# Kernel tuning notes

Hardware: AMD Instinct MI355X
Metric: run time of the kernel (lower is better)

Reference implementation:

```python
import math
import jax, jax.numpy as jnp
import numpy as np

WINDOW = 2  # LocalAttention default window_size
EPS = 1e-6


def _linear(x, W, b):
    return x @ W + b


def local_attention(x, Wq, bq, Wk, bk, Wv, bv):
    # x: [B, S, D]
    B, S, D = x.shape
    q = _linear(x, Wq, bq)
    k = _linear(x, Wk, bk)
    v = _linear(x, Wv, bv)
    idx = jnp.arange(S)
    # 0/1 banded mask -> softmax gives a dense row-stochastic matrix (faithful to source)
    mask = (jnp.abs(idx[:, None] - idx[None, :]) <= WINDOW).astype(x.dtype)  # [S, S]
    A = jax.nn.softmax(mask, axis=-1)  # [S, S]
    kk = jnp.einsum('st,btd->bsd', A, k)  # bmm(A, k)
    scores = jnp.einsum('bsd,btd->bst', q, kk) / math.sqrt(D)
    return jnp.einsum('bst,btd->bsd', jax.nn.softmax(scores, axis=-1), v)


def whole_norm(x, w, b):
    # LayerNorm with normalized_shape == full [B, S, D]: normalize over ALL elements
    mu = jnp.mean(x)
    var = jnp.mean(jnp.square(x - mu))
    return (x - mu) * jax.lax.rsqrt(var + EPS) * w + b


def ffn(x, W1, b1, W2, b2):
    return _linear(jax.nn.relu(_linear(x, W1, b1)), W2, b2)


def branch(feat, Wq, bq, Wk, bk, Wv, bv, W1, b1, W2, b2, nw, nb):
    out = local_attention(feat, Wq, bq, Wk, bk, Wv, bv)
    out = whole_norm(out + feat, nw, nb)
    out = ffn(out, W1, b1, W2, b2)
    return whole_norm(out + feat, nw, nb)


def _make_params(key, B, S, D):
    ks = jax.random.split(key, 5)
    s = 1.0 / math.sqrt(D)
    Wq = jax.random.normal(ks[0], (D, D), jnp.float32) * s
    Wk = jax.random.normal(ks[1], (D, D), jnp.float32) * s
    Wv = jax.random.normal(ks[2], (D, D), jnp.float32) * s
    W1 = jax.random.normal(ks[3], (D, 4 * D), jnp.float32) * s
    W2 = jax.random.normal(ks[4], (4 * D, D), jnp.float32) * (1.0 / math.sqrt(4 * D))
    return dict(Wq=Wq, bq=jnp.zeros((D,)), Wk=Wk, bk=jnp.zeros((D,)),
                Wv=Wv, bv=jnp.zeros((D,)), W1=W1, b1=jnp.zeros((4 * D,)),
                W2=W2, b2=jnp.zeros((D,)), nw=jnp.ones((B, S, D)), nb=jnp.zeros((B, S, D)))


def setup_inputs() -> dict:
    key = jax.random.key(0)
    k0, k1, k2, k3 = jax.random.split(key, 4)
    B, St, Dt = 8, 512, 1024
    Si, Di = 196, 768
    inp = {
        'text_feature': jax.random.normal(k0, (B, St, Dt), jnp.float32),
        'image_feature': jax.random.normal(k1, (B, Si, Di), jnp.float32),
    }
    tp = _make_params(k2, B, St, Dt)
    ip = _make_params(k3, B, Si, Di)
    for k, v in tp.items():
        inp['t_' + k] = v
    for k, v in ip.items():
        inp['i_' + k] = v
    return inp


def reference(text_feature, image_feature,
              t_Wq, t_bq, t_Wk, t_bk, t_Wv, t_bv, t_W1, t_b1, t_W2, t_b2, t_nw, t_nb,
              i_Wq, i_bq, i_Wk, i_bk, i_Wv, i_bv, i_W1, i_b1, i_W2, i_b2, i_nw, i_nb):
    image_out = branch(image_feature, i_Wq, i_bq, i_Wk, i_bk, i_Wv, i_bv,
                       i_W1, i_b1, i_W2, i_b2, i_nw, i_nb)
    text_out = branch(text_feature, t_Wq, t_bq, t_Wk, t_bk, t_Wv, t_bv,
                      t_W1, t_b1, t_W2, t_b2, t_nw, t_nb)
    return (text_out, image_out)
```

## Files before the change

### kernel.cpp

```cpp
#include <hip/hip_runtime.h>
#include <math.h>

typedef float  f32x4  __attribute__((ext_vector_type(4)));
typedef short  bf16x8 __attribute__((ext_vector_type(8)));

__device__ __forceinline__ unsigned short f2bf(float f) {
    union { float f; unsigned u; } v; v.f = f;
    unsigned u = v.u;
    return (unsigned short)((u + 0x7FFFu + ((u >> 16) & 1u)) >> 16);
}
__device__ __forceinline__ float bf2f(unsigned short u) {
    union { unsigned u; float f; } v; v.u = (unsigned)u << 16; return v.f;
}

#define GLOAD_LDS16(g, l)                                                      \
    __builtin_amdgcn_global_load_lds(                                          \
        (const __attribute__((address_space(1))) void*)(g),                    \
        (__attribute__((address_space(3))) void*)(l), 16, 0, 0)

template<int MR, int NR, bool OUT_BF16, bool RELU>
__global__ __launch_bounds__(512, 4)
void gemm2_bf16(const unsigned short* __restrict__ A,
                const unsigned short* __restrict__ BT,
                const float* __restrict__ bias, void* __restrict__ Cv,
                int M, int N, int K, int lda, int ldb, int ldc,
                long long sA, long long sB, long long sC, float alpha,
                int gx, int gy)
{
    constexpr int BK = 32;
    constexpr int WM = MR * 16, WN = NR * 16;
    constexpr int BM = 2 * WM, BN = 4 * WN;
    __shared__ unsigned short Asm[2][BM * BK];
    __shared__ unsigned short Bsm[2][BN * BK];

    A  += (long long)blockIdx.z * sA;
    BT += (long long)blockIdx.z * sB;
    char* Cb = (char*)Cv + (long long)blockIdx.z * sC * (OUT_BF16 ? 2 : 4);

    const int nwg = gx * gy;
    int orig = blockIdx.x;
    int xcd = orig & 7, sidx = orig >> 3;
    int qq = nwg >> 3, rr = nwg & 7;
    int wg = (xcd < rr ? xcd * (qq + 1) : rr * (qq + 1) + (xcd - rr) * qq) + sidx;
    const int row0 = (wg / gx) * BM;
    const int col0 = (wg % gx) * BN;

    const int tid  = threadIdx.x;
    const int lane = tid & 63;
    const int wave = tid >> 6;
    const int wr   = wave >> 2;
    const int wc   = wave & 3;

    const int srow = tid >> 2;
    const int skel = (tid & 3) * 8;

    const int lrow = lane & 15;
    const int lk   = (lane >> 4) * 8;

    f32x4 acc[MR][NR] = {};

    auto stage = [&](int buf, int k0) {
        #pragma unroll
        for (int is = 0; is < BM / 128; ++is)
            GLOAD_LDS16(A + (long long)(row0 + is * 128 + srow) * lda + (k0 + skel),
                        &Asm[buf][(is * 128 + srow) * BK + skel]);
        #pragma unroll
        for (int is = 0; is < BN / 128; ++is)
            GLOAD_LDS16(BT + (long long)(col0 + is * 128 + srow) * ldb + (k0 + skel),
                        &Bsm[buf][(is * 128 + srow) * BK + skel]);
    };

    const int nt = K / BK;
    stage(0, 0);
    __syncthreads();
    int cur = 0;
    for (int t = 0; t < nt; ++t) {
        if (t + 1 < nt) stage(cur ^ 1, (t + 1) * BK);

        bf16x8 af[MR], bfr[NR];
        #pragma unroll
        for (int mf = 0; mf < MR; ++mf)
            af[mf] = *(const bf16x8*)&Asm[cur][(wr * WM + mf * 16 + lrow) * BK + lk];
        #pragma unroll
        for (int nf = 0; nf < NR; ++nf)
            bfr[nf] = *(const bf16x8*)&Bsm[cur][(wc * WN + nf * 16 + lrow) * BK + lk];
        #pragma unroll
        for (int mf = 0; mf < MR; ++mf)
            #pragma unroll
            for (int nf = 0; nf < NR; ++nf)
                acc[mf][nf] = __builtin_amdgcn_mfma_f32_16x16x32_bf16(
                    af[mf], bfr[nf], acc[mf][nf], 0, 0, 0);

        __syncthreads();
        cur ^= 1;
    }

    const int crow = (lane >> 4) * 4;
    const int ccol = lane & 15;
    #pragma unroll
    for (int mf = 0; mf < MR; ++mf) {
        int rbase = row0 + wr * WM + mf * 16 + crow;
        #pragma unroll
        for (int nf = 0; nf < NR; ++nf) {
            int c = col0 + wc * WN + nf * 16 + ccol;
            if (c >= N) continue;
            float bv = bias ? bias[c] : 0.f;
            #pragma unroll
            for (int j = 0; j < 4; ++j) {
                int r = rbase + j;
                if (r >= M) continue;
                float v = acc[mf][nf][j] * alpha + bv;
                if (RELU) v = fmaxf(v, 0.f);
                if (OUT_BF16)
                    ((unsigned short*)Cb)[(long long)r * ldc + c] = f2bf(v);
                else
                    ((float*)Cb)[(long long)r * ldc + c] = v;
            }
        }
    }
}

template<int MR, int NR>
static void gemm2_t(bool outBf16, bool relu,
                    const unsigned short* A, const unsigned short* BT, const float* bias,
                    void* C, int M, int N, int K, int lda, int ldb, int ldc,
                    int batch, long long sA, long long sB, long long sC,
                    float alpha, hipStream_t st)
{
    const int BM = 2 * MR * 16, BN = 4 * NR * 16;
    int gx = (N + BN - 1) / BN, gy = (M + BM - 1) / BM;
    dim3 grid(gx * gy, 1, batch);
    if (outBf16) {
        if (relu) gemm2_bf16<MR, NR, true , true ><<<grid, 512, 0, st>>>(A, BT, bias, C, M, N, K, lda, ldb, ldc, sA, sB, sC, alpha, gx, gy);
        else      gemm2_bf16<MR, NR, true , false><<<grid, 512, 0, st>>>(A, BT, bias, C, M, N, K, lda, ldb, ldc, sA, sB, sC, alpha, gx, gy);
    } else {
        if (relu) gemm2_bf16<MR, NR, false, true ><<<grid, 512, 0, st>>>(A, BT, bias, C, M, N, K, lda, ldb, ldc, sA, sB, sC, alpha, gx, gy);
        else      gemm2_bf16<MR, NR, false, false><<<grid, 512, 0, st>>>(A, BT, bias, C, M, N, K, lda, ldb, ldc, sA, sB, sC, alpha, gx, gy);
    }
}

template<int BM, int BN, bool OUT_BF16>
__global__ __launch_bounds__(256)
void gemm_bf16(const unsigned short* __restrict__ A,
               const unsigned short* __restrict__ BT,
               const float* __restrict__ bias, void* __restrict__ Cv,
               int M, int N, int K, int lda, int ldb, int ldc,
               long long sA, long long sB, long long sC, float alpha,
               int gx, int gy)
{
    constexpr int BK = 32;
    constexpr int WM = BM / 2, WN = BN / 2;
    constexpr int MR = WM / 16, NR = WN / 16;
    __shared__ unsigned short Asm[BM * BK];
    __shared__ unsigned short Bsm[BN * BK];

    A  += (long long)blockIdx.z * sA;
    BT += (long long)blockIdx.z * sB;
    char* Cb = (char*)Cv + (long long)blockIdx.z * sC * (OUT_BF16 ? 2 : 4);

    const int nwg = gx * gy;
    int orig = blockIdx.x;
    int xcd = orig & 7, sidx = orig >> 3;
    int qq = nwg >> 3, rr = nwg & 7;
    int wg = (xcd < rr ? xcd * (qq + 1) : rr * (qq + 1) + (xcd - rr) * qq) + sidx;
    const int row0 = (wg % gy) * BM;
    const int col0 = (wg / gy) * BN;

    const int tid  = threadIdx.x;
    const int lane = tid & 63;
    const int wave = tid >> 6;
    const int wr   = wave >> 1;
    const int wc   = wave & 1;

    const int srow = tid >> 2;
    const int skel = (tid & 3) * 8;

    f32x4 acc[MR][NR] = {};

    const int lrow = lane & 15;
    const int lk   = (lane >> 4) * 8;

    for (int k0 = 0; k0 < K; k0 += BK) {
        #pragma unroll
        for (int is = 0; is < BM / 64; ++is)
            GLOAD_LDS16(A + (long long)(row0 + is * 64 + srow) * lda + (k0 + skel),
                        &Asm[(is * 64 + srow) * BK + skel]);
        #pragma unroll
        for (int is = 0; is < BN / 64; ++is)
            GLOAD_LDS16(BT + (long long)(col0 + is * 64 + srow) * ldb + (k0 + skel),
                        &Bsm[(is * 64 + srow) * BK + skel]);
        __syncthreads();

        bf16x8 af[MR], bfr[NR];
        #pragma unroll
        for (int mf = 0; mf < MR; ++mf)
            af[mf] = *(const bf16x8*)&Asm[(wr * WM + mf * 16 + lrow) * BK + lk];
        #pragma unroll
        for (int nf = 0; nf < NR; ++nf)
            bfr[nf] = *(const bf16x8*)&Bsm[(wc * WN + nf * 16 + lrow) * BK + lk];
        #pragma unroll
        for (int mf = 0; mf < MR; ++mf)
            #pragma unroll
            for (int nf = 0; nf < NR; ++nf)
                acc[mf][nf] = __builtin_amdgcn_mfma_f32_16x16x32_bf16(
                    af[mf], bfr[nf], acc[mf][nf], 0, 0, 0);
        __syncthreads();
    }

    const int crow = (lane >> 4) * 4;
    const int ccol = lane & 15;
    #pragma unroll
    for (int mf = 0; mf < MR; ++mf) {
        int rbase = row0 + wr * WM + mf * 16 + crow;
        #pragma unroll
        for (int nf = 0; nf < NR; ++nf) {
            int c = col0 + wc * WN + nf * 16 + ccol;
            if (c >= N) continue;
            float bv = bias ? bias[c] : 0.f;
            #pragma unroll
            for (int j = 0; j < 4; ++j) {
                int r = rbase + j;
                if (r >= M) continue;
                float v = acc[mf][nf][j] * alpha + bv;
                if (OUT_BF16)
                    ((unsigned short*)Cb)[(long long)r * ldc + c] = f2bf(v);
                else
                    ((float*)Cb)[(long long)r * ldc + c] = v;
            }
        }
    }
}

template<int BM, int BN>
static void gemm_t(bool outBf16,
                   const unsigned short* A, const unsigned short* BT, const float* bias,
                   void* C, int M, int N, int K, int lda, int ldb, int ldc,
                   int batch, long long sA, long long sB, long long sC,
                   float alpha, hipStream_t st)
{
    int gx = (N + BN - 1) / BN, gy = (M + BM - 1) / BM;
    dim3 grid(gx * gy, 1, batch);
    if (outBf16)
        gemm_bf16<BM, BN, true ><<<grid, 256, 0, st>>>(A, BT, bias, C, M, N, K, lda, ldb, ldc, sA, sB, sC, alpha, gx, gy);
    else
        gemm_bf16<BM, BN, false><<<grid, 256, 0, st>>>(A, BT, bias, C, M, N, K, lda, ldb, ldc, sA, sB, sC, alpha, gx, gy);
}

__global__ void splitk_stats_kernel(const float4* __restrict__ part,
                                    const float4* __restrict__ bias,
                                    const float4* __restrict__ x,
                                    float4* __restrict__ z,
                                    double* __restrict__ dpart,
                                    long long n4, int N4, int nsplit, long long stride4)
{
    __shared__ double rs[256], rs2[256];
    int tid = threadIdx.x;
    long long i = (long long)blockIdx.x * blockDim.x + tid;
    long long gs = (long long)gridDim.x * blockDim.x;
    double s = 0.0, s2 = 0.0;
    for (; i < n4; i += gs) {
        float4 a = part[i];
        for (int sp = 1; sp < nsplit; ++sp) {
            float4 b = part[(long long)sp * stride4 + i];
            a.x += b.x; a.y += b.y; a.z += b.z; a.w += b.w;
        }
        float4 bv = bias[(int)(i % N4)];
        float4 xv = x[i];
        a.x += bv.x + xv.x; a.y += bv.y + xv.y; a.z += bv.z + xv.z; a.w += bv.w + xv.w;
        z[i] = a;
        s  += (double)a.x + (double)a.y + (double)a.z + (double)a.w;
        s2 += (double)a.x * a.x + (double)a.y * a.y + (double)a.z * a.z + (double)a.w * a.w;
    }
    rs[tid] = s; rs2[tid] = s2; __syncthreads();
    for (int k = 128; k > 0; k >>= 1) {
        if (tid < k) { rs[tid] += rs[tid + k]; rs2[tid] += rs2[tid + k]; }
        __syncthreads();
    }
    if (tid == 0) { dpart[2 * blockIdx.x] = rs[0]; dpart[2 * blockIdx.x + 1] = rs2[0]; }
}

__global__ void norm_apply_z_kernel(const float4* __restrict__ z,
                                    const float4* __restrict__ nw, const float4* __restrict__ nb,
                                    const float* __restrict__ stats, float4* __restrict__ out,
                                    long long n4)
{
    float mu = stats[0], rstd = stats[1];
    long long i = (long long)blockIdx.x * blockDim.x + threadIdx.x;
    long long stride = (long long)gridDim.x * blockDim.x;
    for (; i < n4; i += stride) {
        float4 zv = z[i], wv = nw[i], bv = nb[i];
        float4 o;
        o.x = (zv.x - mu) * rstd * wv.x + bv.x;
        o.y = (zv.y - mu) * rstd * wv.y + bv.y;
        o.z = (zv.z - mu) * rstd * wv.z + bv.z;
        o.w = (zv.w - mu) * rstd * wv.w + bv.w;
        out[i] = o;
    }
}

__global__ void cast_bf16_kernel(const float4* __restrict__ in,
                                 ushort4* __restrict__ out, long long n4)
{
    long long i = (long long)blockIdx.x * blockDim.x + threadIdx.x;
    long long stride = (long long)gridDim.x * blockDim.x;
    for (; i < n4; i += stride) {
        float4 v = in[i];
        ushort4 o;
        o.x = f2bf(v.x); o.y = f2bf(v.y); o.z = f2bf(v.z); o.w = f2bf(v.w);
        out[i] = o;
    }
}

__global__ void transpose_cast_kernel(const float* __restrict__ src,
                                      unsigned short* __restrict__ dst,
                                      int R, int C, int Rpad,
                                      long long sSrc, long long sDst)
{
    __shared__ float t[32][33];
    src += (long long)blockIdx.z * sSrc;
    dst += (long long)blockIdx.z * sDst;
    int r0 = blockIdx.x * 32, c0 = blockIdx.y * 32;
    int tx = threadIdx.x & 31, ty = threadIdx.x >> 5;
    #pragma unroll
    for (int i = 0; i < 32; i += 8) {
        int r = r0 + ty + i, c = c0 + tx;
        t[ty + i][tx] = (r < R && c < C) ? src[(long long)r * C + c] : 0.f;
    }
    __syncthreads();
    #pragma unroll
    for (int i = 0; i < 32; i += 8) {
        int c = c0 + ty + i, r = r0 + tx;
        if (c < C && r < Rpad)
            dst[(long long)c * Rpad + r] = f2bf(t[tx][ty + i]);
    }
}

__global__ void transpose_bf16_kernel(const unsigned short* __restrict__ src,
                                      unsigned short* __restrict__ dst,
                                      int R, int C, int Rpad, int ldS,
                                      long long sSrc, long long sDst)
{
    __shared__ unsigned short t[32][33];
    src += (long long)blockIdx.z * sSrc;
    dst += (long long)blockIdx.z * sDst;
    int r0 = blockIdx.x * 32, c0 = blockIdx.y * 32;
    int tx = threadIdx.x & 31, ty = threadIdx.x >> 5;
    #pragma unroll
    for (int i = 0; i < 32; i += 8) {
        int r = r0 + ty + i, c = c0 + tx;
        t[ty + i][tx] = (r < R && c < C) ? src[(long long)r * ldS + c] : (unsigned short)0;
    }
    __syncthreads();
    #pragma unroll
    for (int i = 0; i < 32; i += 8) {
        int c = c0 + ty + i, r = r0 + tx;
        if (c < C && r < Rpad)
            dst[(long long)c * Rpad + r] = t[tx][ty + i];
    }
}

#define KTOT_NCH 16
__global__ void ktot_partial_bf16(const unsigned short* __restrict__ k,
                                  float* __restrict__ part,
                                  int B, int S, int D, int ld)
{
    int bch = blockIdx.x;
    int b  = bch / KTOT_NCH;
    int ch = bch % KTOT_NCH;
    int d  = blockIdx.y * 256 + threadIdx.x;
    if (d >= D) return;
    int len = (S + KTOT_NCH - 1) / KTOT_NCH;
    int lo = ch * len;
    int hi = lo + len < S ? lo + len : S;
    const unsigned short* kp = k + ((long long)b * S + lo) * ld + d;
    float s = 0.f;
    for (int t = lo; t < hi; ++t, kp += ld) s += bf2f(*kp);
    part[(long long)bch * D + d] = s;
}

__global__ void ktot_finish_kernel(const float* __restrict__ part,
                                   float* __restrict__ ktot, int B, int D)
{
    int idx = blockIdx.x * blockDim.x + threadIdx.x;
    if (idx >= B * D) return;
    int b = idx / D, d = idx % D;
    float s = 0.f;
    #pragma unroll
    for (int ch = 0; ch < KTOT_NCH; ++ch)
        s += part[((long long)b * KTOT_NCH + ch) * D + d];
    ktot[idx] = s;
}

__global__ void kk_bf16_kernel(const unsigned short* __restrict__ k,
                               const float* __restrict__ ktot,
                               unsigned short* __restrict__ kk,
                               int B, int S, int D, int ld)
{
    long long idx = (long long)blockIdx.x * blockDim.x + threadIdx.x;
    int D4 = D >> 2;
    long long n4 = (long long)B * S * D4;
    if (idx >= n4) return;
    int d4 = (int)(idx % D4);
    long long bs = idx / D4;
    int s = (int)(bs % S);
    int b = (int)(bs / S);
    int lo = s - 2 > 0 ? s - 2 : 0;
    int hi = s + 2 < S - 1 ? s + 2 : S - 1;
    int c = hi - lo + 1;
    const float E = 2.718281828459045f;
    float Zinv = 1.f / ((float)(S - c) + E * (float)c);

    float w0 = 0.f, w1 = 0.f, w2 = 0.f, w3 = 0.f;
    const unsigned short* kp = k + ((long long)b * S + lo) * ld + d4 * 4;
    for (int t = lo; t <= hi; ++t, kp += ld) {
        ushort4 kv = *(const ushort4*)kp;
        w0 += bf2f(kv.x); w1 += bf2f(kv.y); w2 += bf2f(kv.z); w3 += bf2f(kv.w);
    }
    float4 tot = *((const float4*)(ktot + b * D) + d4);
    ushort4 o;
    o.x = f2bf((tot.x + (E - 1.f) * w0) * Zinv);
    o.y = f2bf((tot.y + (E - 1.f) * w1) * Zinv);
    o.z = f2bf((tot.z + (E - 1.f) * w2) * Zinv);
    o.w = f2bf((tot.w + (E - 1.f) * w3) * Zinv);
    ((ushort4*)(kk + ((long long)b * S + s) * D))[d4] = o;
}

__global__ void softmax_rows_bf16(const float* __restrict__ sc,
                                  unsigned short* __restrict__ P, int S, int Spad)
{
    long long row = blockIdx.x;
    const float* p = sc + row * (long long)Spad;
    unsigned short* o = P + row * (long long)Spad;
    int tid = threadIdx.x;
    __shared__ float red[256];

    float m = -INFINITY;
    for (int t = tid; t < S; t += 256) m = fmaxf(m, p[t]);
    red[tid] = m; __syncthreads();
    for (int s = 128; s > 0; s >>= 1) {
        if (tid < s) red[tid] = fmaxf(red[tid], red[tid + s]);
        __syncthreads();
    }
    m = red[0];
    __syncthreads();

    float sum = 0.f;
    for (int t = tid; t < S; t += 256) sum += __expf(p[t] - m);
    red[tid] = sum; __syncthreads();
    for (int s = 128; s > 0; s >>= 1) {
        if (tid < s) red[tid] += red[tid + s];
        __syncthreads();
    }
    float inv = 1.f / red[0];
    for (int t = tid; t < Spad; t += 256)
        o[t] = (t < S) ? f2bf(__expf(p[t] - m) * inv) : (unsigned short)0;
}

__global__ void stats_kernel(const float4* __restrict__ a, const float4* __restrict__ f,
                             double* __restrict__ part, long long n4)
{
    __shared__ double rs[256], rs2[256];
    int tid = threadIdx.x;
    long long i = (long long)blockIdx.x * blockDim.x + tid;
    long long stride = (long long)gridDim.x * blockDim.x;
    double s = 0.0, s2 = 0.0;
    for (; i < n4; i += stride) {
        float4 av = a[i], fv = f[i];
        float z0 = av.x + fv.x, z1 = av.y + fv.y, z2 = av.z + fv.z, z3 = av.w + fv.w;
        s  += (double)z0 + (double)z1 + (double)z2 + (double)z3;
        s2 += (double)z0 * z0 + (double)z1 * z1 + (double)z2 * z2 + (double)z3 * z3;
    }
    rs[tid] = s; rs2[tid] = s2; __syncthreads();
    for (int k = 128; k > 0; k >>= 1) {
        if (tid < k) { rs[tid] += rs[tid + k]; rs2[tid] += rs2[tid + k]; }
        __syncthreads();
    }
    if (tid == 0) { part[2 * blockIdx.x] = rs[0]; part[2 * blockIdx.x + 1] = rs2[0]; }
}

__global__ void finish_stats(const double* __restrict__ part, int npart,
                             float* __restrict__ stats, double n)
{
    __shared__ double rs[256], rs2[256];
    int tid = threadIdx.x;
    double s = 0.0, s2 = 0.0;
    for (int i = tid; i < npart; i += 256) { s += part[2 * i]; s2 += part[2 * i + 1]; }
    rs[tid] = s; rs2[tid] = s2; __syncthreads();
    for (int k = 128; k > 0; k >>= 1) {
        if (tid < k) { rs[tid] += rs[tid + k]; rs2[tid] += rs2[tid + k]; }
        __syncthreads();
    }
    if (tid == 0) {
        double mu  = rs[0] / n;
        double var = rs2[0] / n - mu * mu;
        stats[0] = (float)mu;
        stats[1] = (float)(1.0 / sqrt(var + 1e-6));
    }
}

__global__ void norm_apply_kernel(const float4* __restrict__ a, const float4* __restrict__ f,
                                  const float4* __restrict__ nw, const float4* __restrict__ nb,
                                  const float* __restrict__ stats, ushort4* __restrict__ out,
                                  long long n4)
{
    float mu = stats[0], rstd = stats[1];
    long long i = (long long)blockIdx.x * blockDim.x + threadIdx.x;
    long long stride = (long long)gridDim.x * blockDim.x;
    for (; i < n4; i += stride) {
        float4 av = a[i], fv = f[i], wv = nw[i], bv = nb[i];
        ushort4 o;
        o.x = f2bf((av.x + fv.x - mu) * rstd * wv.x + bv.x);
        o.y = f2bf((av.y + fv.y - mu) * rstd * wv.y + bv.y);
        o.z = f2bf((av.z + fv.z - mu) * rstd * wv.z + bv.z);
        o.w = f2bf((av.w + fv.w - mu) * rstd * wv.w + bv.w);
        out[i] = o;
    }
}

struct Bufs {
    unsigned short *xb, *qkv, *kkb, *vT, *P, *h, *WqkvT, *W1T, *W2T;
    float *f32buf, *bqkv, *ktot, *ktot_part, *stats;
    double *part;
};

static void run_branch(const float* x, const float* const* w, bool big,
                       float* out, int B, int S, int D, const Bufs& wsb, hipStream_t st)
{
    const float *Wq = w[0], *bq = w[1], *Wk = w[2], *bk = w[3], *Wv = w[4], *bv = w[5];
    const float *W1 = w[6], *b1 = w[7], *W2 = w[8], *b2 = w[9], *nw = w[10], *nb = w[11];

    const int Spad = (S + 31) & ~31;
    const long long M = (long long)B * S;
    const long long n = M * D;
    const long long n4 = n / 4;
    const float inv_sqrt_d = (float)(1.0 / sqrt((double)D));
    const int D3 = 3 * D, D4 = 4 * D;

    unsigned short* y1b = wsb.kkb;
    float* scores = (float*)wsb.h;
    float* splitbuf = (float*)wsb.qkv;

    cast_bf16_kernel<<<1024, 256, 0, st>>>((const float4*)x, (ushort4*)wsb.xb, n4);
    transpose_cast_kernel<<<dim3((D + 31) / 32, (D + 31) / 32, 1), 256, 0, st>>>(Wq, wsb.WqkvT,               D, D, D, 0, 0);
    transpose_cast_kernel<<<dim3((D + 31) / 32, (D + 31) / 32, 1), 256, 0, st>>>(Wk, wsb.WqkvT + (long long)D * D, D, D, D, 0, 0);
    transpose_cast_kernel<<<dim3((D + 31) / 32, (D + 31) / 32, 1), 256, 0, st>>>(Wv, wsb.WqkvT + 2LL * D * D, D, D, D, 0, 0);
    transpose_cast_kernel<<<dim3((D + 31) / 32, (D4 + 31) / 32, 1), 256, 0, st>>>(W1, wsb.W1T, D, D4, D, 0, 0);
    transpose_cast_kernel<<<dim3((D4 + 31) / 32, (D + 31) / 32, 1), 256, 0, st>>>(W2, wsb.W2T, D4, D, D4, 0, 0);
    hipMemcpyAsync(wsb.bqkv,         bq, D * sizeof(float), hipMemcpyDeviceToDevice, st);
    hipMemcpyAsync(wsb.bqkv + D,     bk, D * sizeof(float), hipMemcpyDeviceToDevice, st);
    hipMemcpyAsync(wsb.bqkv + 2 * D, bv, D * sizeof(float), hipMemcpyDeviceToDevice, st);

    gemm2_t<4, 2>(true, false, wsb.xb, wsb.WqkvT, wsb.bqkv, wsb.qkv,
                  (int)M, D3, D, D, D, D3, 1, 0, 0, 0, 1.f, st);

    const unsigned short* kcol = wsb.qkv + D;
    ktot_partial_bf16<<<dim3(B * KTOT_NCH, (D + 255) / 256), 256, 0, st>>>(kcol, wsb.ktot_part, B, S, D, D3);
    ktot_finish_kernel<<<(B * D + 255) / 256, 256, 0, st>>>(wsb.ktot_part, wsb.ktot, B, D);
    kk_bf16_kernel<<<(int)((n4 + 255) / 256), 256, 0, st>>>(kcol, wsb.ktot, wsb.kkb, B, S, D, D3);

    transpose_bf16_kernel<<<dim3((Spad + 31) / 32, (D + 31) / 32, B), 256, 0, st>>>(
        wsb.qkv + 2 * D, wsb.vT, S, D, Spad, D3, (long long)S * D3, (long long)D * Spad);

    gemm_t<64, 64>(false, wsb.qkv, wsb.kkb, nullptr, scores, S, S, D, D3, D, Spad,
                   B, (long long)S * D3, (long long)S * D, (long long)S * Spad, inv_sqrt_d, st);
    softmax_rows_bf16<<<(int)M, 256, 0, st>>>(scores, wsb.P, S, Spad);

    gemm_t<128, 64>(false, wsb.P, wsb.vT, nullptr, wsb.f32buf, S, D, Spad, Spad, Spad, D,
                    B, (long long)S * Spad, (long long)D * Spad, (long long)S * D, 1.f, st);

    stats_kernel<<<1024, 256, 0, st>>>((const float4*)wsb.f32buf, (const float4*)x, wsb.part, n4);
    finish_stats<<<1, 256, 0, st>>>(wsb.part, 1024, wsb.stats, (double)n);
    norm_apply_kernel<<<2048, 256, 0, st>>>((const float4*)wsb.f32buf, (const float4*)x,
        (const float4*)nw, (const float4*)nb, wsb.stats, (ushort4*)y1b, n4);

    gemm2_t<4, 2>(true, true, y1b, wsb.W1T, b1, wsb.h, (int)M, D4, D, D, D, D4, 1, 0, 0, 0, 1.f, st);

    {
        int nsplit = big ? 2 : 4;
        int Ksp = D4 / nsplit;
        gemm2_t<4, 2>(false, false, wsb.h, wsb.W2T, nullptr, splitbuf,
                      (int)M, D, Ksp, D4, D4, D,
                      nsplit, Ksp, Ksp, M * D, 1.f, st);
        splitk_stats_kernel<<<1024, 256, 0, st>>>((const float4*)splitbuf, (const float4*)b2,
                                                  (const float4*)x, (float4*)wsb.f32buf,
                                                  wsb.part, n4, D / 4, nsplit, n4);
        finish_stats<<<1, 256, 0, st>>>(wsb.part, 1024, wsb.stats, (double)n);
        norm_apply_z_kernel<<<2048, 256, 0, st>>>((const float4*)wsb.f32buf,
            (const float4*)nw, (const float4*)nb, wsb.stats, (float4*)out, n4);
    }
}

extern "C" void kernel_launch(void* const* d_in, const int* in_sizes, int n_in,
                              void* d_out, int out_size, void* d_ws, size_t ws_size,
                              hipStream_t stream)
{
    const float* text  = (const float*)d_in[0];
    const float* image = (const float*)d_in[1];
    const float* tw[12];
    const float* iw[12];
    for (int i = 0; i < 12; ++i) tw[i] = (const float*)d_in[2 + i];
    for (int i = 0; i < 12; ++i) iw[i] = (const float*)d_in[14 + i];

    float* out_text = (float*)d_out;
    float* out_img  = out_text + 8LL * 512 * 1024;

    char* p = (char*)d_ws;
    auto alloc = [&](long long bytes) {
        char* r = p;
        p += (bytes + 255) & ~255LL;
        return r;
    };
    const long long MD  = 4096LL * 1024;
    const long long BDS = 8LL * 1024 * 512;
    const long long SS  = 8LL * 512 * 512;
    Bufs b;
    b.xb      = (unsigned short*)alloc(MD * 2);
    b.qkv     = (unsigned short*)alloc(MD * 3 * 2);
    b.kkb     = (unsigned short*)alloc(MD * 2);
    b.vT      = (unsigned short*)alloc(BDS * 2);
    b.P       = (unsigned short*)alloc(SS * 2);
    b.h       = (unsigned short*)alloc(MD * 4 * 2);
    b.WqkvT   = (unsigned short*)alloc(3LL * 1024 * 1024 * 2);
    b.W1T     = (unsigned short*)alloc(4096LL * 1024 * 2);
    b.W2T     = (unsigned short*)alloc(4096LL * 1024 * 2);
    b.f32buf  = (float*)alloc(MD * 4);
    b.bqkv    = (float*)alloc(3LL * 1024 * 4);
    b.ktot    = (float*)alloc(8192LL * 4);
    b.ktot_part = (float*)alloc(8192LL * KTOT_NCH * 4);
    b.part    = (double*)alloc(2048LL * 8);
    b.stats   = (float*)alloc(256);

    run_branch(text,  tw, true,  out_text, 8, 512, 1024, b, stream);
    run_branch(image, iw, false, out_img,  8, 196, 768,  b, stream);
}
```

Before: 460.3 us.

## Deepen GEMM K-tile to 64 with XOR-swizzled LDS and raised MFMA priority

The main bf16 GEMM kernel now stages 64-wide K tiles instead of 32, which halves the number of barrier iterations per output tile. The shared-memory layout uses an XOR swizzle on 16-byte chunks to avoid LDS bank conflicts when fragments are read. It also raises wave priority around the MFMA block and increases split-K for the small image branch from 4 to 8. The costs are doubled LDS use per block, which may lower occupancy under the 4-blocks launch bound, and a larger split-K reduction buffer for the image branch.

```diff
diff --git a/kernel.cpp b/kernel.cpp
--- a/kernel.cpp
+++ b/kernel.cpp
@@ -20,14 +20,14 @@
 
 template<int MR, int NR, bool OUT_BF16, bool RELU>
 __global__ __launch_bounds__(512, 4)
-void gemm2_bf16(const unsigned short* __restrict__ A,
+void gemm4_bf16(const unsigned short* __restrict__ A,
                 const unsigned short* __restrict__ BT,
                 const float* __restrict__ bias, void* __restrict__ Cv,
                 int M, int N, int K, int lda, int ldb, int ldc,
                 long long sA, long long sB, long long sC, float alpha,
                 int gx, int gy)
 {
-    constexpr int BK = 32;
+    constexpr int BK = 64;
     constexpr int WM = MR * 16, WN = NR * 16;
     constexpr int BM = 2 * WM, BN = 4 * WN;
     __shared__ unsigned short Asm[2][BM * BK];
@@ -51,51 +51,65 @@
     const int wr   = wave >> 2;
     const int wc   = wave & 3;
 
-    const int srow = tid >> 2;
-    const int skel = (tid & 3) * 8;
-
     const int lrow = lane & 15;
-    const int lk   = (lane >> 4) * 8;
+    const int cgrp = lane >> 4;
 
     f32x4 acc[MR][NR] = {};
 
+    const int srl = tid >> 3;
+    const int scl = (tid & 7) ^ (srl & 7);
+
     auto stage = [&](int buf, int k0) {
         #pragma unroll
-        for (int is = 0; is < BM / 128; ++is)
-            GLOAD_LDS16(A + (long long)(row0 + is * 128 + srow) * lda + (k0 + skel),
-                        &Asm[buf][(is * 128 + srow) * BK + skel]);
-        #pragma unroll
-        for (int is = 0; is < BN / 128; ++is)
-            GLOAD_LDS16(BT + (long long)(col0 + is * 128 + srow) * ldb + (k0 + skel),
-                        &Bsm[buf][(is * 128 + srow) * BK + skel]);
+        for (int is = 0; is < BM / 64; ++is)
+            GLOAD_LDS16(A + (long long)(row0 + is * 64 + srl) * lda + (k0 + scl * 8),
+                        &Asm[buf][is * 64 * BK + tid * 8]);
+        #pragma unroll
+        for (int is = 0; is < BN / 64; ++is)
+            GLOAD_LDS16(BT + (long long)(col0 + is * 64 + srl) * ldb + (k0 + scl * 8),
+                        &Bsm[buf][is * 64 * BK + tid * 8]);
     };
 
     const int nt = K / BK;
     stage(0, 0);
     __syncthreads();
-    int cur = 0;
+
     for (int t = 0; t < nt; ++t) {
-        if (t + 1 < nt) stage(cur ^ 1, (t + 1) * BK);
-
-        bf16x8 af[MR], bfr[NR];
-        #pragma unroll
-        for (int mf = 0; mf < MR; ++mf)
-            af[mf] = *(const bf16x8*)&Asm[cur][(wr * WM + mf * 16 + lrow) * BK + lk];
-        #pragma unroll
-        for (int nf = 0; nf < NR; ++nf)
-            bfr[nf] = *(const bf16x8*)&Bsm[cur][(wc * WN + nf * 16 + lrow) * BK + lk];
-        #pragma unroll
-        for (int mf = 0; mf < MR; ++mf)
+        if (t + 1 < nt) stage((t + 1) & 1, (t + 1) * BK);
+        const int cur = t & 1;
+
+        bf16x8 a_[2][MR], b_[2][NR];
+        #pragma unroll
+        for (int kk = 0; kk < 2; ++kk) {
             #pragma unroll
-            for (int nf = 0; nf < NR; ++nf)
-                acc[mf][nf] = __builtin_amdgcn_mfma_f32_16x16x32_bf16(
-                    af[mf], bfr[nf], acc[mf][nf], 0, 0, 0);
-
-        __syncthreads();
-        cur ^= 1;
-    }
-
-    const int crow = (lane >> 4) * 4;
+            for (int mf = 0; mf < MR; ++mf) {
+                int row = wr * WM + mf * 16 + lrow;
+                int phys = (kk * 4 + cgrp) ^ (row & 7);
+                a_[kk][mf] = *(const bf16x8*)&Asm[cur][row * BK + phys * 8];
+            }
+            #pragma unroll
+            for (int nf = 0; nf < NR; ++nf) {
+                int row = wc * WN + nf * 16 + lrow;
+                int phys = (kk * 4 + cgrp) ^ (row & 7);
+                b_[kk][nf] = *(const bf16x8*)&Bsm[cur][row * BK + phys * 8];
+            }
+        }
+
+        __builtin_amdgcn_s_setprio(1);
+        #pragma unroll
+        for (int kk = 0; kk < 2; ++kk)
+            #pragma unroll
+            for (int mf = 0; mf < MR; ++mf)
+                #pragma unroll
+                for (int nf = 0; nf < NR; ++nf)
+                    acc[mf][nf] = __builtin_amdgcn_mfma_f32_16x16x32_bf16(
+                        a_[kk][mf], b_[kk][nf], acc[mf][nf], 0, 0, 0);
+        __builtin_amdgcn_s_setprio(0);
+
+        __syncthreads();
+    }
+
+    const int crow = cgrp * 4;
     const int ccol = lane & 15;
     #pragma unroll
     for (int mf = 0; mf < MR; ++mf) {
@@ -121,7 +135,7 @@
 }
 
 template<int MR, int NR>
-static void gemm2_t(bool outBf16, bool relu,
+static void gemm4_t(bool outBf16, bool relu,
                     const unsigned short* A, const unsigned short* BT, const float* bias,
                     void* C, int M, int N, int K, int lda, int ldb, int ldc,
                     int batch, long long sA, long long sB, long long sC,
@@ -131,11 +145,11 @@
     int gx = (N + BN - 1) / BN, gy = (M + BM - 1) / BM;
     dim3 grid(gx * gy, 1, batch);
     if (outBf16) {
-        if (relu) gemm2_bf16<MR, NR, true , true ><<<grid, 512, 0, st>>>(A, BT, bias, C, M, N, K, lda, ldb, ldc, sA, sB, sC, alpha, gx, gy);
-        else      gemm2_bf16<MR, NR, true , false><<<grid, 512, 0, st>>>(A, BT, bias, C, M, N, K, lda, ldb, ldc, sA, sB, sC, alpha, gx, gy);
+        if (relu) gemm4_bf16<MR, NR, true , true ><<<grid, 512, 0, st>>>(A, BT, bias, C, M, N, K, lda, ldb, ldc, sA, sB, sC, alpha, gx, gy);
+        else      gemm4_bf16<MR, NR, true , false><<<grid, 512, 0, st>>>(A, BT, bias, C, M, N, K, lda, ldb, ldc, sA, sB, sC, alpha, gx, gy);
     } else {
-        if (relu) gemm2_bf16<MR, NR, false, true ><<<grid, 512, 0, st>>>(A, BT, bias, C, M, N, K, lda, ldb, ldc, sA, sB, sC, alpha, gx, gy);
-        else      gemm2_bf16<MR, NR, false, false><<<grid, 512, 0, st>>>(A, BT, bias, C, M, N, K, lda, ldb, ldc, sA, sB, sC, alpha, gx, gy);
+        if (relu) gemm4_bf16<MR, NR, false, true ><<<grid, 512, 0, st>>>(A, BT, bias, C, M, N, K, lda, ldb, ldc, sA, sB, sC, alpha, gx, gy);
+        else      gemm4_bf16<MR, NR, false, false><<<grid, 512, 0, st>>>(A, BT, bias, C, M, N, K, lda, ldb, ldc, sA, sB, sC, alpha, gx, gy);
     }
 }
 
@@ -550,7 +564,7 @@
     hipMemcpyAsync(wsb.bqkv + D,     bk, D * sizeof(float), hipMemcpyDeviceToDevice, st);
     hipMemcpyAsync(wsb.bqkv + 2 * D, bv, D * sizeof(float), hipMemcpyDeviceToDevice, st);
 
-    gemm2_t<4, 2>(true, false, wsb.xb, wsb.WqkvT, wsb.bqkv, wsb.qkv,
+    gemm4_t<4, 2>(true, false, wsb.xb, wsb.WqkvT, wsb.bqkv, wsb.qkv,
                   (int)M, D3, D, D, D, D3, 1, 0, 0, 0, 1.f, st);
 
     const unsigned short* kcol = wsb.qkv + D;
@@ -573,12 +587,12 @@
     norm_apply_kernel<<<2048, 256, 0, st>>>((const float4*)wsb.f32buf, (const float4*)x,
         (const float4*)nw, (const float4*)nb, wsb.stats, (ushort4*)y1b, n4);
 
-    gemm2_t<4, 2>(true, true, y1b, wsb.W1T, b1, wsb.h, (int)M, D4, D, D, D, D4, 1, 0, 0, 0, 1.f, st);
+    gemm4_t<4, 2>(true, true, y1b, wsb.W1T, b1, wsb.h, (int)M, D4, D, D, D, D4, 1, 0, 0, 0, 1.f, st);
 
     {
-        int nsplit = big ? 2 : 4;
+        int nsplit = big ? 2 : 8;
         int Ksp = D4 / nsplit;
-        gemm2_t<4, 2>(false, false, wsb.h, wsb.W2T, nullptr, splitbuf,
+        gemm4_t<4, 2>(false, false, wsb.h, wsb.W2T, nullptr, splitbuf,
                       (int)M, D, Ksp, D4, D4, D,
                       nsplit, Ksp, Ksp, M * D, 1.f, st);
         splitk_stats_kernel<<<1024, 256, 0, st>>>((const float4*)splitbuf, (const float4*)b2,
```

Result: no change. 455.5 us (-1.0%).
